# Optimization experiments

Hardware: AMD Instinct MI355X
Metric: run time of the kernel (lower is better)

The kernel has to match this reference:

```python
import jax, jax.numpy as jnp
import numpy as np

B, IN_DIM, OUT_DIM, N_WIN, N_SEQ, N_REAL = 4, 8, 64, 64, 4096, 6144


def setup_inputs() -> dict:
    key = jax.random.key(0)
    k1, k2, k3, k4 = jax.random.split(key, 4)
    x = jax.random.normal(k1, (B, IN_DIM, N_SEQ), dtype=jnp.float32)
    bound = 1.0 / np.sqrt(IN_DIM * N_WIN)  # torch uniform init bound k=1/(inDim*nWin)
    weight = jax.random.uniform(k2, (OUT_DIM, IN_DIM, N_WIN), jnp.float32, -bound, bound)
    bias = jax.random.uniform(k3, (OUT_DIM,), jnp.float32, -bound, bound)
    # sorted, unique onset indices per batch (irregular but monotone, in-range)
    ks = jax.random.split(k4, B)
    sourceIdx = jax.vmap(
        lambda k: jnp.sort(jax.random.choice(k, N_REAL, (N_SEQ,), replace=False))
    )(ks).astype(jnp.int32)
    return {"x": x, "weight": weight, "bias": bias,
            "sourceIdx": sourceIdx, "nRealLen": N_REAL}


def reference(x, weight, bias, sourceIdx, nRealLen):
    # LTITRFGen (ifAddBiasInForward=False): broadcast-mul + sum over inDim
    # == einsum over the stimulus-feature axis.
    TRFs = jnp.einsum('bis,oiw->bows', x, weight)  # (B, outDim, nWin, nSeq)
    Bz, O, W, S = TRFs.shape

    # TRFAligner: scatter TRFs into zero cache at per-sample source indices
    def scatter_one(trf_b, idx_b):  # trf_b: (O, W, S), idx_b: (S,)
        return jnp.zeros((O, W, nRealLen), trf_b.dtype).at[:, :, idx_b].set(trf_b)

    cache = jax.vmap(scatter_one)(TRFs, sourceIdx)  # (B, O, W, nRealLen)

    # torch fold with kernel (nWin,1) == overlap-add along the lag axis:
    # out[b,o,t] = sum_w cache[b,o,w,t-w]
    out = jnp.zeros((Bz, O, nRealLen + W - 1), TRFs.dtype)
    for w in range(W):  # static small lag loop (nWin=64)
        out = out.at[:, :, w:w + nRealLen].add(cache[:, :, w])

    # crop to nRealLen and add per-channel LTI bias (ifEnableUserTRFGen=False path)
    return out[:, :, :nRealLen] + bias[None, :, None]
```

## Files before the change

kernel.cpp:

```cpp
#include <hip/hip_runtime.h>
#include <hip/hip_bf16.h>

#define BB 4
#define IN_DIM 8
#define OUT_DIM 64
#define N_WIN 64
#define N_SEQ 4096
#define N_REAL 6144

typedef __attribute__((ext_vector_type(8)))  short short8;
typedef __attribute__((ext_vector_type(16))) float floatx16;

static __device__ __forceinline__ unsigned short f2bf(float f) {
    union { float f; unsigned int u; } v; v.f = f;
    unsigned int r = v.u + 0x7fffu + ((v.u >> 16) & 1u);
    return (unsigned short)(r >> 16);
}

__global__ __launch_bounds__(256)
void k_wprep(const float* __restrict__ w, unsigned short* __restrict__ w2)
{
    const int tg = blockIdx.x * 256 + threadIdx.x;
    const int l = tg >> 6, o = tg & 63;
    const float* wp = w + (size_t)o * (IN_DIM * N_WIN) + l;
    unsigned short v[8];
    #pragma unroll
    for (int i = 0; i < 8; ++i) v[i] = f2bf(wp[(size_t)i * N_WIN]);
    uint4 pk;
    pk.x = v[0] | ((unsigned)v[1] << 16); pk.y = v[2] | ((unsigned)v[3] << 16);
    pk.z = v[4] | ((unsigned)v[5] << 16); pk.w = v[6] | ((unsigned)v[7] << 16);
    *(uint4*)(w2 + ((size_t)(l * OUT_DIM + o)) * 8) = pk;
}

__global__ __launch_bounds__(128)
void k_gemm(const float* __restrict__ x, const unsigned short* __restrict__ w2,
            const float* __restrict__ bias, const int* __restrict__ sidx,
            float* __restrict__ out)
{
    __shared__ unsigned short zlds[96 * 8];

    const int tid = threadIdx.x;
    const int t0  = blockIdx.x * 32;
    const int b   = blockIdx.y;

    unsigned int* zw = (unsigned int*)zlds;
    zw[tid] = 0u; zw[tid + 128] = 0u; zw[tid + 256] = 0u;

    const int* idxb = sidx + b * N_SEQ;
    const int vlo = t0 - 63;
    int lo = 0, hi = N_SEQ;
    while (lo < hi) { int m = (lo + hi) >> 1; if (idxb[m] < vlo) lo = m + 1; else hi = m; }

    __syncthreads();

    if (tid < 96) {
        int s = lo + tid;
        if (s < N_SEQ) {
            int r = idxb[s] - vlo;
            if ((unsigned)r < 96u) {
                const float* xp = x + (size_t)b * IN_DIM * N_SEQ + s;
                unsigned short v[8];
                #pragma unroll
                for (int i = 0; i < 8; ++i) v[i] = f2bf(xp[(size_t)i * N_SEQ]);
                uint4 pk;
                pk.x = v[0] | ((unsigned)v[1] << 16); pk.y = v[2] | ((unsigned)v[3] << 16);
                pk.z = v[4] | ((unsigned)v[5] << 16); pk.w = v[6] | ((unsigned)v[7] << 16);
                *(uint4*)(zlds + r * 8) = pk;
            }
        }
    }
    __syncthreads();

    const int mh = tid >> 6;
    const int ln = tid & 31;
    const int lq = (tid >> 5) & 1;

    floatx16 acc = {};
    const short8* wv = (const short8*)w2;
    const short8* zv = (const short8*)zlds;

    #pragma unroll 8
    for (int ks = 0; ks < 32; ++ks) {
        const int l = 2 * ks + lq;
        short8 a  = wv[l * OUT_DIM + mh * 32 + ln];
        short8 bz = zv[ln + 63 - l];
        acc = __builtin_amdgcn_mfma_f32_32x32x16_bf16(a, bz, acc, 0, 0, 0);
    }

    #pragma unroll
    for (int p = 0; p < 16; ++p) {
        int o = (p & 3) + 8 * (p >> 2) + 4 * lq + mh * 32;
        out[((size_t)b * OUT_DIM + o) * N_REAL + t0 + ln] = acc[p] + bias[o];
    }
}

extern "C" void kernel_launch(void* const* d_in, const int* in_sizes, int n_in,
                              void* d_out, int out_size, void* d_ws, size_t ws_size,
                              hipStream_t stream) {
    const float* px = nullptr; const float* pw = nullptr;
    const float* pb = nullptr; const int* ps = nullptr;

    for (int i = 0; i < n_in; ++i) {
        switch (in_sizes[i]) {
            case BB * IN_DIM * N_SEQ:        px = (const float*)d_in[i]; break;
            case OUT_DIM * IN_DIM * N_WIN:   pw = (const float*)d_in[i]; break;
            case OUT_DIM:                    pb = (const float*)d_in[i]; break;
            case BB * N_SEQ:                 ps = (const int*)d_in[i];   break;
            default: break;
        }
    }
    if (!px || !pw || !pb || !ps) {
        px = (const float*)d_in[0]; pw = (const float*)d_in[1];
        pb = (const float*)d_in[2]; ps = (const int*)d_in[3];
    }

    unsigned short* w2 = (unsigned short*)d_ws;
    float* out = (float*)d_out;

    k_wprep<<<16, 256, 0, stream>>>(pw, w2);
    k_gemm<<<dim3(N_REAL / 32, BB), 128, 0, stream>>>(px, w2, pb, ps, out);
}
```

Baseline: 72.93 us.

## Precompute per-tile search bounds in prep kernel and restructure gather with weight prefetch

```diff
diff --git a/kernel.cpp b/kernel.cpp
--- a/kernel.cpp
+++ b/kernel.cpp
@@ -7,6 +7,7 @@
 #define N_WIN 64
 #define N_SEQ 4096
 #define N_REAL 6144
+#define NTB (N_REAL / 32)
 
 typedef __attribute__((ext_vector_type(8)))  short short8;
 typedef __attribute__((ext_vector_type(16))) float floatx16;
@@ -18,7 +19,8 @@
 }
 
 __global__ __launch_bounds__(256)
-void k_wprep(const float* __restrict__ w, unsigned short* __restrict__ w2)
+void k_prep(const float* __restrict__ w, const int* __restrict__ sidx,
+            unsigned short* __restrict__ w2, int* __restrict__ lob)
 {
     const int tg = blockIdx.x * 256 + threadIdx.x;
     const int l = tg >> 6, o = tg & 63;
@@ -30,59 +32,70 @@
     pk.x = v[0] | ((unsigned)v[1] << 16); pk.y = v[2] | ((unsigned)v[3] << 16);
     pk.z = v[4] | ((unsigned)v[5] << 16); pk.w = v[6] | ((unsigned)v[7] << 16);
     *(uint4*)(w2 + ((size_t)(l * OUT_DIM + o)) * 8) = pk;
+
+    if (tg < BB * NTB) {
+        const int b  = tg / NTB, bx = tg - b * NTB;
+        const int vlo = bx * 32 - 63;
+        const int* idxb = sidx + b * N_SEQ;
+        int lo = 0, hi = N_SEQ;
+        while (lo < hi) { int m = (lo + hi) >> 1; if (idxb[m] < vlo) lo = m + 1; else hi = m; }
+        lob[tg] = lo;
+    }
 }
 
 __global__ __launch_bounds__(128)
 void k_gemm(const float* __restrict__ x, const unsigned short* __restrict__ w2,
             const float* __restrict__ bias, const int* __restrict__ sidx,
-            float* __restrict__ out)
+            const int* __restrict__ lob, float* __restrict__ out)
 {
     __shared__ unsigned short zlds[96 * 8];
 
     const int tid = threadIdx.x;
-    const int t0  = blockIdx.x * 32;
+    const int bx  = blockIdx.x;
     const int b   = blockIdx.y;
+    const int t0  = bx * 32;
+    const int vlo = t0 - 63;
+    const int lo  = lob[b * NTB + bx];
 
     unsigned int* zw = (unsigned int*)zlds;
     zw[tid] = 0u; zw[tid + 128] = 0u; zw[tid + 256] = 0u;
 
+    const int ig = tid >> 4;
+    const int sl = tid & 15;
     const int* idxb = sidx + b * N_SEQ;
-    const int vlo = t0 - 63;
-    int lo = 0, hi = N_SEQ;
-    while (lo < hi) { int m = (lo + hi) >> 1; if (idxb[m] < vlo) lo = m + 1; else hi = m; }
-
-    __syncthreads();
-
-    if (tid < 96) {
-        int s = lo + tid;
-        if (s < N_SEQ) {
-            int r = idxb[s] - vlo;
-            if ((unsigned)r < 96u) {
-                const float* xp = x + (size_t)b * IN_DIM * N_SEQ + s;
-                unsigned short v[8];
-                #pragma unroll
-                for (int i = 0; i < 8; ++i) v[i] = f2bf(xp[(size_t)i * N_SEQ]);
-                uint4 pk;
-                pk.x = v[0] | ((unsigned)v[1] << 16); pk.y = v[2] | ((unsigned)v[3] << 16);
-                pk.z = v[4] | ((unsigned)v[5] << 16); pk.w = v[6] | ((unsigned)v[7] << 16);
-                *(uint4*)(zlds + r * 8) = pk;
-            }
-        }
+    const float* xb = x + ((size_t)b * IN_DIM + ig) * N_SEQ;
+    int   rarr[6]; float xv[6];
+    #pragma unroll
+    for (int c = 0; c < 6; ++c) {
+        int s = lo + c * 16 + sl;
+        bool valid = (s < N_SEQ);
+        rarr[c] = valid ? (idxb[s] - vlo) : -1;
+        xv[c]   = valid ? xb[s] : 0.f;
     }
-    __syncthreads();
 
     const int mh = tid >> 6;
     const int ln = tid & 31;
     const int lq = (tid >> 5) & 1;
+    const short8* wv = (const short8*)w2;
+    short8 apre[8];
+    #pragma unroll
+    for (int k = 0; k < 8; ++k)
+        apre[k] = wv[(2 * k + lq) * OUT_DIM + mh * 32 + ln];
+
+    __syncthreads();
+    #pragma unroll
+    for (int c = 0; c < 6; ++c)
+        if ((unsigned)rarr[c] < 96u)
+            zlds[rarr[c] * 8 + ig] = f2bf(xv[c]);
+    __syncthreads();
 
     floatx16 acc = {};
-    const short8* wv = (const short8*)w2;
     const short8* zv = (const short8*)zlds;
-
-    #pragma unroll 8
+    #pragma unroll
     for (int ks = 0; ks < 32; ++ks) {
         const int l = 2 * ks + lq;
-        short8 a  = wv[l * OUT_DIM + mh * 32 + ln];
+        short8 a  = (ks < 8) ? apre[ks]
+                             : wv[l * OUT_DIM + mh * 32 + ln];
         short8 bz = zv[ln + 63 - l];
         acc = __builtin_amdgcn_mfma_f32_32x32x16_bf16(a, bz, acc, 0, 0, 0);
     }
@@ -115,8 +128,9 @@
     }
 
     unsigned short* w2 = (unsigned short*)d_ws;
+    int* lob = (int*)((char*)d_ws + 64 * 1024);
     float* out = (float*)d_out;
 
-    k_wprep<<<16, 256, 0, stream>>>(pw, w2);
-    k_gemm<<<dim3(N_REAL / 32, BB), 128, 0, stream>>>(px, w2, pb, ps, out);
+    k_prep<<<16, 256, 0, stream>>>(pw, ps, w2, lob);
+    k_gemm<<<dim3(NTB, BB), 128, 0, stream>>>(px, w2, pb, ps, lob, out);
 }
```

Result: no change. 72.22 us (median of 2 runs) (-1.0%).
